# Performance work log

Measured on AMD Instinct MI355X. Metric: run time of the kernel, lower is better.

## Reference

```python
import jax, jax.numpy as jnp
import numpy as np

DIM = 1024
NUM_HEADS = 16
HEAD_DIM = DIM // NUM_HEADS
SCALE = HEAD_DIM ** -0.5


def setup_inputs() -> dict:
    key = jax.random.key(0)
    k1, k2, k3 = jax.random.split(key, 3)
    B, N = 4, 2048
    x = jax.random.normal(k1, (B, N, DIM), dtype=jnp.float32)
    w_qkv = jax.random.normal(k2, (DIM, 3 * DIM), dtype=jnp.float32) * (DIM ** -0.5)
    w_proj = jax.random.normal(k3, (DIM, DIM), dtype=jnp.float32) * (DIM ** -0.5)
    b_proj = jnp.zeros((DIM,), dtype=jnp.float32)
    return {"x": x, "w_qkv": w_qkv, "w_proj": w_proj, "b_proj": b_proj}


def reference(x, w_qkv, w_proj, b_proj):
    B, N, C = x.shape
    H, D = NUM_HEADS, HEAD_DIM
    # qkv projection: (B,N,3C) -> (3,B,H,N,D)
    qkv = (x @ w_qkv).reshape(B, N, 3, H, D).transpose(2, 0, 3, 1, 4)
    q, k, v = qkv[0], qkv[1], qkv[2]
    # full attention scores (B,H,N,N), scaled
    attn = jnp.einsum("bhnd,bhmd->bhnm", q, k) * SCALE
    attn = jax.nn.softmax(attn, axis=-1)
    out = jnp.einsum("bhnm,bhmd->bhnd", attn, v)
    out = out.transpose(0, 2, 1, 3).reshape(B, N, C)
    return out @ w_proj + b_proj
```

## Files before the change

### kernel.cpp

```cpp
#include <hip/hip_runtime.h>
#include <stdint.h>

#define DIM 1024
#define NHEADS 16
#define HDIM 64
#define BATCH 4
#define SEQ 2048
#define NTOK (BATCH*SEQ)
#define SCALE_L2E 0.1803368801111244f

typedef float f32x4  __attribute__((ext_vector_type(4)));
typedef short s16x8  __attribute__((ext_vector_type(8)));

#define MFMA16(a,b,c) __builtin_amdgcn_mfma_f32_16x16x32_bf16((a),(b),(c),0,0,0)

static __device__ __forceinline__ uint16_t f2bf(float f) {
    uint32_t u = __builtin_bit_cast(uint32_t, f);
    return (uint16_t)((u + 0x7FFFu + ((u >> 16) & 1u)) >> 16);
}

static __device__ __forceinline__ uint32_t cvt_pk_bf16(float lo, float hi) {
    uint32_t r;
    asm("v_cvt_pk_bf16_f32 %0, %1, %2" : "=v"(r) : "v"(lo), "v"(hi));
    return r;
}

static __device__ __forceinline__ void gl_lds16(const void* g, void* l) {
    __builtin_amdgcn_global_load_lds(
        (const __attribute__((address_space(1))) unsigned int*)g,
        (__attribute__((address_space(3))) unsigned int*)l, 16, 0, 0);
}

__global__ void convert_f32_bf16(const float* __restrict__ in, uint16_t* __restrict__ out) {
    const int i = blockIdx.x * blockDim.x + threadIdx.x;
    const float4 a = ((const float4*)in)[2*i];
    const float4 b = ((const float4*)in)[2*i + 1];
    ushort4 lo, hi;
    lo.x = f2bf(a.x); lo.y = f2bf(a.y); lo.z = f2bf(a.z); lo.w = f2bf(a.w);
    hi.x = f2bf(b.x); hi.y = f2bf(b.y); hi.z = f2bf(b.z); hi.w = f2bf(b.w);
    ((ushort4*)out)[2*i]     = lo;
    ((ushort4*)out)[2*i + 1] = hi;
}

__global__ void transpose_conv(const float* __restrict__ w, uint16_t* __restrict__ wT,
                               int K, int N) {
    __shared__ float t[32][33];
    const int tx = threadIdx.x, ty = threadIdx.y;
    const int n0 = blockIdx.x * 32, k0 = blockIdx.y * 32;
    #pragma unroll
    for (int i = 0; i < 4; ++i)
        t[ty + i*8][tx] = w[(size_t)(k0 + ty + i*8) * N + n0 + tx];
    __syncthreads();
    #pragma unroll
    for (int i = 0; i < 4; ++i)
        wT[(size_t)(n0 + ty + i*8) * K + k0 + tx] = f2bf(t[tx][ty + i*8]);
}

template <int MODE>
__global__ __launch_bounds__(256) void gemm_bt(
    const uint16_t* __restrict__ A, const uint16_t* __restrict__ B,
    void* __restrict__ C, const float* __restrict__ bias,
    int M, int N, int K)
{
    __shared__ uint16_t As[128*64];
    __shared__ uint16_t Bs[128*64];
    const int tid  = threadIdx.x;
    const int lane = tid & 63;
    const int wid  = tid >> 6;
    const int wm = wid >> 1, wn = wid & 1;
    const long row0 = (long)blockIdx.y * 128;
    const long col0 = (long)blockIdx.x * 128;

    const int sr  = lane >> 3;
    const int scb = (lane & 7) * 16;

    f32x4 acc[4][4] = {};

    for (int kt = 0; kt < K; kt += 64) {
        #pragma unroll
        for (int j = 0; j < 4; ++j) {
            const int r = (wid*4 + j)*8 + sr;
            const int c = (scb ^ ((r & 7) << 4)) >> 1;
            gl_lds16(&A[(row0 + r)*K + kt + c], &As[(wid*4 + j)*512]);
            gl_lds16(&B[(col0 + r)*K + kt + c], &Bs[(wid*4 + j)*512]);
        }
        __syncthreads();
        #pragma unroll
        for (int ks = 0; ks < 2; ++ks) {
            const int xb = (ks*32 + (lane >> 4)*8) * 2;
            s16x8 av[4], bv[4];
            #pragma unroll
            for (int f = 0; f < 4; ++f) {
                const int ra = wm*64 + f*16 + (lane & 15);
                av[f] = *(const s16x8*)((const char*)As + ra*128 + (xb ^ ((ra & 7) << 4)));
                const int rb = wn*64 + f*16 + (lane & 15);
                bv[f] = *(const s16x8*)((const char*)Bs + rb*128 + (xb ^ ((rb & 7) << 4)));
            }
            #pragma unroll
            for (int i = 0; i < 4; ++i)
                #pragma unroll
                for (int j = 0; j < 4; ++j)
                    acc[i][j] = MFMA16(av[i], bv[j], acc[i][j]);
        }
        __syncthreads();
    }

    #pragma unroll
    for (int i = 0; i < 4; ++i) {
        const long row = row0 + wm*64 + i*16 + (lane >> 4)*4;
        #pragma unroll
        for (int j = 0; j < 4; ++j) {
            const long col = col0 + wn*64 + j*16 + (lane & 15);
            #pragma unroll
            for (int r = 0; r < 4; ++r) {
                if (MODE == 0)
                    ((uint16_t*)C)[(row + r)*N + col] = f2bf(acc[i][j][r]);
                else
                    ((float*)C)[(row + r)*N + col] = acc[i][j][r] + bias[col];
            }
        }
    }
}

__global__ __launch_bounds__(512, 2) void qkv_gemm(
    const uint16_t* __restrict__ A, const uint16_t* __restrict__ B,
    uint16_t* __restrict__ Qb, uint16_t* __restrict__ Kb,
    uint16_t* __restrict__ VTb)
{
    __shared__ uint16_t As[2][256*64];
    __shared__ uint16_t Bs[2][192*64];
    const int tid = threadIdx.x, lane = tid & 63, wid = tid >> 6;
    const int wr = wid >> 2, wc = wid & 3;
    const int q15 = lane & 15, g = lane >> 4;

    int bid = blockIdx.y * gridDim.x + blockIdx.x;
    bid = (bid & 7) * 64 + (bid >> 3);
    const int  bx  = bid & 15;
    const long row0 = (long)(bid >> 4) * 256;
    const int  col0 = bx * 192;

    const int r_  = tid >> 3;
    const int sc  = (((tid & 7) * 16) ^ ((r_ & 7) << 4)) >> 1;

    f32x4 acc[8][3] = {};

#define QSTAGE(bf_, t_) do {                                                    \
    const int kt_ = (t_) * 64;                                                  \
    _Pragma("unroll")                                                           \
    for (int j_ = 0; j_ < 4; ++j_)                                              \
        gl_lds16(&A[(row0 + j_*64 + r_)*DIM + kt_ + sc], &As[bf_][j_*4096 + tid*8]); \
    _Pragma("unroll")                                                           \
    for (int j_ = 0; j_ < 3; ++j_)                                              \
        gl_lds16(&B[(size_t)(col0 + j_*64 + r_)*DIM + kt_ + sc], &Bs[bf_][j_*4096 + tid*8]); \
} while (0)

    QSTAGE(0, 0);

    for (int t = 0; t < 16; ++t) {
        const int p = t & 1;
        __syncthreads();
        QSTAGE(p ^ 1, (t < 15 ? t + 1 : 15));
        #pragma unroll
        for (int ks = 0; ks < 2; ++ks) {
            const int xb = (ks*32 + g*8) * 2;
            s16x8 av[8], bv[3];
            #pragma unroll
            for (int m = 0; m < 8; ++m) {
                const int ra = wr*128 + m*16 + q15;
                av[m] = *(const s16x8*)((const char*)As[p] + ra*128 + (xb ^ ((ra & 7) << 4)));
            }
            #pragma unroll
            for (int n = 0; n < 3; ++n) {
                const int rb = wc*48 + n*16 + q15;
                bv[n] = *(const s16x8*)((const char*)Bs[p] + rb*128 + (xb ^ ((rb & 7) << 4)));
            }
            #pragma unroll
            for (int m = 0; m < 8; ++m)
                #pragma unroll
                for (int n = 0; n < 3; ++n)
                    acc[m][n] = MFMA16(av[m], bv[n], acc[m][n]);
        }
    }
#undef QSTAGE

    #pragma unroll
    for (int n = 0; n < 3; ++n) {
        const int c = col0 + wc*48 + n*16 + q15;
        const int s = c >> 10;
        if (s == 2) {
            const int vrow = c - 2048;
            #pragma unroll
            for (int m = 0; m < 8; ++m) {
                const long rr = row0 + wr*128 + m*16 + g*4;
                uint2 w;
                w.x = cvt_pk_bf16(acc[m][n][0], acc[m][n][1]);
                w.y = cvt_pk_bf16(acc[m][n][2], acc[m][n][3]);
                *(uint2*)&VTb[(size_t)vrow*NTOK + rr] = w;
            }
        } else {
            uint16_t* dst = s ? Kb : Qb;
            const float scl = s ? 1.0f : SCALE_L2E;
            const int hd = (c >> 6) & 15, d = c & 63;
            #pragma unroll
            for (int m = 0; m < 8; ++m) {
                #pragma unroll
                for (int r = 0; r < 4; ++r) {
                    const long rr = row0 + wr*128 + m*16 + g*4 + r;
                    const int b = (int)(rr >> 11), nt = (int)(rr & 2047);
                    dst[((size_t)(b*NHEADS + hd)*SEQ + nt)*HDIM + d] = f2bf(acc[m][n][r] * scl);
                }
            }
        }
    }
}

__global__ __launch_bounds__(256) void attn_kernel(
    const uint16_t* __restrict__ Q, const uint16_t* __restrict__ Kg,
    const uint16_t* __restrict__ VT, uint16_t* __restrict__ O)
{
    __shared__ uint16_t Ks[2][64*64];
    __shared__ uint16_t Vs[2][64*64];
    __shared__ uint16_t Ps[128*64];
    const int tid = threadIdx.x, lane = tid & 63, wid = tid >> 6;
    const int bid = blockIdx.x;
    const int xcd = bid & 7, idx = bid >> 3;
    const int bh = xcd*8 + (idx >> 4);
    const int qt = idx & 15;
    const int b = bh >> 4, h = bh & 15;
    const uint16_t* Qh = Q  + (size_t)bh * SEQ * HDIM;
    const uint16_t* Kh = Kg + (size_t)bh * SEQ * HDIM;
    const uint16_t* Vh = VT + (size_t)h * HDIM * NTOK + (size_t)b * SEQ;
    const int qbase = qt*128 + wid*32;
    const int g = lane >> 4, q15 = lane & 15;
    const int swl = (lane & 7) << 4;

    s16x8 bq[2][2];
    #pragma unroll
    for (int i = 0; i < 2; ++i)
        #pragma unroll
        for (int ks = 0; ks < 2; ++ks)
            bq[i][ks] = *(const s16x8*)&Qh[(size_t)(qbase + i*16 + q15)*HDIM + ks*32 + g*8];

    f32x4 o[2][4] = {};
    f32x4 lacc[2] = {};

    const int sr  = lane >> 3;
    const int scb = (lane & 7) * 16;
    const int stg_c = (scb ^ (sr << 4)) >> 1;

    #define STAGE(bf, t)                                                          \
        _Pragma("unroll")                                                         \
        for (int j = 0; j < 2; ++j) {                                             \
            const int r = (wid*2 + j)*8 + sr;                                     \
            gl_lds16(&Kh[(size_t)((t)*64 + r)*HDIM + stg_c], &Ks[bf][(wid*2 + j)*512]); \
            gl_lds16(&Vh[(size_t)r*NTOK + (t)*64 + stg_c],   &Vs[bf][(wid*2 + j)*512]); \
        }

    STAGE(0, 0)
    __syncthreads();

    for (int it = 0; it < 32; ++it) {
        const int cur = it & 1;
        if (it < 31) STAGE(cur ^ 1, it + 1)

        const char* ksb = (const char*)Ks[cur];
        const char* vsb = (const char*)Vs[cur];

        f32x4 st[2][4] = {};
        #pragma unroll
        for (int ks = 0; ks < 2; ++ks) {
            const int xb = (ks*32 + g*8) * 2;
            s16x8 ak[4];
            #pragma unroll
            for (int f = 0; f < 4; ++f) {
                const int rk = f*16 + q15;
                ak[f] = *(const s16x8*)(ksb + rk*128 + (xb ^ ((rk & 7) << 4)));
            }
            #pragma unroll
            for (int i = 0; i < 2; ++i)
                #pragma unroll
                for (int f = 0; f < 4; ++f)
                    st[i][f] = MFMA16(ak[f], bq[i][ks], st[i][f]);
        }

        #pragma unroll
        for (int i = 0; i < 2; ++i) {
            #pragma unroll
            for (int f = 0; f < 4; ++f) {
                #pragma unroll
                for (int r = 0; r < 4; ++r)
                    st[i][f][r] = __builtin_amdgcn_exp2f(st[i][f][r]);
            }
            lacc[i] += (st[i][0] + st[i][1]) + (st[i][2] + st[i][3]);
        }

        #pragma unroll
        for (int i = 0; i < 2; ++i) {
            char* base = (char*)Ps + (wid*32 + i*16 + q15)*128;
            #pragma unroll
            for (int f = 0; f < 4; ++f) {
                uint2 w;
                w.x = cvt_pk_bf16(st[i][f][0], st[i][f][1]);
                w.y = cvt_pk_bf16(st[i][f][2], st[i][f][3]);
                *(uint2*)(base + ((f*32 + g*8) ^ swl)) = w;
            }
        }

        #pragma unroll
        for (int ks = 0; ks < 2; ++ks) {
            s16x8 pa[2], vb[4];
            #pragma unroll
            for (int i = 0; i < 2; ++i)
                pa[i] = *(const s16x8*)((const char*)Ps + (wid*32 + i*16 + q15)*128
                                         + ((ks*64 + g*16) ^ swl));
            const int xbv = (ks*32 + g*8) * 2;
            #pragma unroll
            for (int f = 0; f < 4; ++f) {
                const int rv = f*16 + q15;
                vb[f] = *(const s16x8*)(vsb + rv*128 + (xbv ^ ((rv & 7) << 4)));
            }
            #pragma unroll
            for (int i = 0; i < 2; ++i)
                #pragma unroll
                for (int f = 0; f < 4; ++f)
                    o[i][f] = MFMA16(pa[i], vb[f], o[i][f]);
        }

        __syncthreads();
    }
    #undef STAGE

    #pragma unroll
    for (int i = 0; i < 2; ++i) {
        float ls = (lacc[i][0] + lacc[i][1]) + (lacc[i][2] + lacc[i][3]);
        ls += __shfl_xor(ls, 16);
        ls += __shfl_xor(ls, 32);
        #pragma unroll
        for (int r = 0; r < 4; ++r) {
            const float l_r = __shfl(ls, g*4 + r);
            const float inv = 1.0f / l_r;
            const int n = qbase + i*16 + g*4 + r;
            const size_t base = ((size_t)b*SEQ + n)*DIM + h*HDIM;
            #pragma unroll
            for (int f = 0; f < 4; ++f)
                O[base + f*16 + q15] = f2bf(o[i][f][r] * inv);
        }
    }
}

extern "C" void kernel_launch(void* const* d_in, const int* in_sizes, int n_in,
                              void* d_out, int out_size, void* d_ws, size_t ws_size,
                              hipStream_t stream)
{
    const float* x      = (const float*)d_in[0];
    const float* w_qkv  = (const float*)d_in[1];
    const float* w_proj = (const float*)d_in[2];
    const float* b_proj = (const float*)d_in[3];
    float* out = (float*)d_out;

    uint16_t* xb     = (uint16_t*)d_ws;
    uint16_t* wqkvT  = xb     + (size_t)NTOK*DIM;
    uint16_t* wprojT = wqkvT  + (size_t)3*DIM*DIM;
    uint16_t* Qb     = wprojT + (size_t)DIM*DIM;
    uint16_t* Kb     = Qb     + (size_t)NTOK*DIM;
    uint16_t* VTb    = Kb     + (size_t)NTOK*DIM;
    uint16_t* attn_o = VTb    + (size_t)NTOK*DIM;

    convert_f32_bf16<<<dim3(NTOK*DIM/8/256), dim3(256), 0, stream>>>(x, xb);
    transpose_conv<<<dim3(96, 32), dim3(32, 8), 0, stream>>>(w_qkv, wqkvT, DIM, 3*DIM);
    transpose_conv<<<dim3(32, 32), dim3(32, 8), 0, stream>>>(w_proj, wprojT, DIM, DIM);
    qkv_gemm<<<dim3(16, 32), dim3(512), 0, stream>>>(xb, wqkvT, Qb, Kb, VTb);
    attn_kernel<<<dim3(1024), dim3(256), 0, stream>>>(Qb, Kb, VTb, attn_o);
    gemm_bt<1><<<dim3(8, 64), dim3(256), 0, stream>>>(attn_o, wprojT, out, b_proj, NTOK, DIM, DIM);
}
```

Measured before the change: 199.4 us.

## Merge weight transposes, enlarge attention blocks, add double-buffered projection GEMM

Merges the two weight transpose launches into one kernel. The attention kernel now uses 512-thread blocks covering 256 queries each, so every K/V tile staged in shared memory serves twice as many queries and each thread issues a single staging load. The generic output-projection GEMM is replaced by a 256x128-tile kernel that double-buffers its shared-memory tiles. The qkv_gemm launch bound drops its min-blocks hint, so the compiler may use more registers at the cost of fewer resident blocks. The larger tiles cut global traffic but halve the block count to 512 for attention and 256 for projection, which may reduce occupancy.

Result: faster. 187.2 us (-6.1%).

```diff
diff --git a/kernel.cpp b/kernel.cpp
--- a/kernel.cpp
+++ b/kernel.cpp
@@ -42,87 +42,25 @@
     ((ushort4*)out)[2*i + 1] = hi;
 }
 
-__global__ void transpose_conv(const float* __restrict__ w, uint16_t* __restrict__ wT,
-                               int K, int N) {
+__global__ void transpose_conv2(const float* __restrict__ w_qkv, uint16_t* __restrict__ wqkvT,
+                                const float* __restrict__ w_proj, uint16_t* __restrict__ wprojT) {
     __shared__ float t[32][33];
     const int tx = threadIdx.x, ty = threadIdx.y;
-    const int n0 = blockIdx.x * 32, k0 = blockIdx.y * 32;
+    const int bx = blockIdx.x;
+    const float* w; uint16_t* wT; int N, n0;
+    if (bx < 96) { w = w_qkv;  wT = wqkvT;  N = 3*DIM; n0 = bx * 32; }
+    else         { w = w_proj; wT = wprojT; N = DIM;   n0 = (bx - 96) * 32; }
+    const int k0 = blockIdx.y * 32;
     #pragma unroll
     for (int i = 0; i < 4; ++i)
         t[ty + i*8][tx] = w[(size_t)(k0 + ty + i*8) * N + n0 + tx];
     __syncthreads();
     #pragma unroll
     for (int i = 0; i < 4; ++i)
-        wT[(size_t)(n0 + ty + i*8) * K + k0 + tx] = f2bf(t[tx][ty + i*8]);
-}
-
-template <int MODE>
-__global__ __launch_bounds__(256) void gemm_bt(
-    const uint16_t* __restrict__ A, const uint16_t* __restrict__ B,
-    void* __restrict__ C, const float* __restrict__ bias,
-    int M, int N, int K)
-{
-    __shared__ uint16_t As[128*64];
-    __shared__ uint16_t Bs[128*64];
-    const int tid  = threadIdx.x;
-    const int lane = tid & 63;
-    const int wid  = tid >> 6;
-    const int wm = wid >> 1, wn = wid & 1;
-    const long row0 = (long)blockIdx.y * 128;
-    const long col0 = (long)blockIdx.x * 128;
-
-    const int sr  = lane >> 3;
-    const int scb = (lane & 7) * 16;
-
-    f32x4 acc[4][4] = {};
-
-    for (int kt = 0; kt < K; kt += 64) {
-        #pragma unroll
-        for (int j = 0; j < 4; ++j) {
-            const int r = (wid*4 + j)*8 + sr;
-            const int c = (scb ^ ((r & 7) << 4)) >> 1;
-            gl_lds16(&A[(row0 + r)*K + kt + c], &As[(wid*4 + j)*512]);
-            gl_lds16(&B[(col0 + r)*K + kt + c], &Bs[(wid*4 + j)*512]);
-        }
-        __syncthreads();
-        #pragma unroll
-        for (int ks = 0; ks < 2; ++ks) {
-            const int xb = (ks*32 + (lane >> 4)*8) * 2;
-            s16x8 av[4], bv[4];
-            #pragma unroll
-            for (int f = 0; f < 4; ++f) {
-                const int ra = wm*64 + f*16 + (lane & 15);
-                av[f] = *(const s16x8*)((const char*)As + ra*128 + (xb ^ ((ra & 7) << 4)));
-                const int rb = wn*64 + f*16 + (lane & 15);
-                bv[f] = *(const s16x8*)((const char*)Bs + rb*128 + (xb ^ ((rb & 7) << 4)));
-            }
-            #pragma unroll
-            for (int i = 0; i < 4; ++i)
-                #pragma unroll
-                for (int j = 0; j < 4; ++j)
-                    acc[i][j] = MFMA16(av[i], bv[j], acc[i][j]);
-        }
-        __syncthreads();
-    }
-
-    #pragma unroll
-    for (int i = 0; i < 4; ++i) {
-        const long row = row0 + wm*64 + i*16 + (lane >> 4)*4;
-        #pragma unroll
-        for (int j = 0; j < 4; ++j) {
-            const long col = col0 + wn*64 + j*16 + (lane & 15);
-            #pragma unroll
-            for (int r = 0; r < 4; ++r) {
-                if (MODE == 0)
-                    ((uint16_t*)C)[(row + r)*N + col] = f2bf(acc[i][j][r]);
-                else
-                    ((float*)C)[(row + r)*N + col] = acc[i][j][r] + bias[col];
-            }
-        }
-    }
-}
-
-__global__ __launch_bounds__(512, 2) void qkv_gemm(
+        wT[(size_t)(n0 + ty + i*8) * DIM + k0 + tx] = f2bf(t[tx][ty + i*8]);
+}
+
+__global__ __launch_bounds__(512) void qkv_gemm(
     const uint16_t* __restrict__ A, const uint16_t* __restrict__ B,
     uint16_t* __restrict__ Qb, uint16_t* __restrict__ Kb,
     uint16_t* __restrict__ VTb)
@@ -214,23 +152,93 @@
     }
 }
 
-__global__ __launch_bounds__(256) void attn_kernel(
+__global__ __launch_bounds__(512) void gemm_proj(
+    const uint16_t* __restrict__ A, const uint16_t* __restrict__ B,
+    float* __restrict__ C, const float* __restrict__ bias)
+{
+    __shared__ uint16_t As[2][256*64];
+    __shared__ uint16_t Bs[2][128*64];
+    const int tid = threadIdx.x, lane = tid & 63, wid = tid >> 6;
+    const int wr = wid >> 2, wc = wid & 3;
+    const int q15 = lane & 15, g = lane >> 4;
+    const long row0 = (long)blockIdx.y * 256;
+    const int  col0 = blockIdx.x * 128;
+
+    const int r_  = tid >> 3;
+    const int sc  = (((tid & 7) * 16) ^ ((r_ & 7) << 4)) >> 1;
+
+    f32x4 acc[8][2] = {};
+
+#define PSTAGE(bf_, t_) do {                                                    \
+    const int kt_ = (t_) * 64;                                                  \
+    _Pragma("unroll")                                                           \
+    for (int j_ = 0; j_ < 4; ++j_)                                              \
+        gl_lds16(&A[(row0 + j_*64 + r_)*DIM + kt_ + sc], &As[bf_][j_*4096 + tid*8]); \
+    _Pragma("unroll")                                                           \
+    for (int j_ = 0; j_ < 2; ++j_)                                              \
+        gl_lds16(&B[(size_t)(col0 + j_*64 + r_)*DIM + kt_ + sc], &Bs[bf_][j_*4096 + tid*8]); \
+} while (0)
+
+    PSTAGE(0, 0);
+
+    for (int t = 0; t < 16; ++t) {
+        const int p = t & 1;
+        __syncthreads();
+        PSTAGE(p ^ 1, (t < 15 ? t + 1 : 15));
+        #pragma unroll
+        for (int ks = 0; ks < 2; ++ks) {
+            const int xb = (ks*32 + g*8) * 2;
+            s16x8 av[8], bv[2];
+            #pragma unroll
+            for (int m = 0; m < 8; ++m) {
+                const int ra = wr*128 + m*16 + q15;
+                av[m] = *(const s16x8*)((const char*)As[p] + ra*128 + (xb ^ ((ra & 7) << 4)));
+            }
+            #pragma unroll
+            for (int n = 0; n < 2; ++n) {
+                const int rb = wc*32 + n*16 + q15;
+                bv[n] = *(const s16x8*)((const char*)Bs[p] + rb*128 + (xb ^ ((rb & 7) << 4)));
+            }
+            #pragma unroll
+            for (int m = 0; m < 8; ++m)
+                #pragma unroll
+                for (int n = 0; n < 2; ++n)
+                    acc[m][n] = MFMA16(av[m], bv[n], acc[m][n]);
+        }
+    }
+#undef PSTAGE
+
+    #pragma unroll
+    for (int n = 0; n < 2; ++n) {
+        const int col = col0 + wc*32 + n*16 + q15;
+        const float bval = bias[col];
+        #pragma unroll
+        for (int m = 0; m < 8; ++m) {
+            const long row = row0 + wr*128 + m*16 + g*4;
+            #pragma unroll
+            for (int r = 0; r < 4; ++r)
+                C[(row + r)*DIM + col] = acc[m][n][r] + bval;
+        }
+    }
+}
+
+__global__ __launch_bounds__(512) void attn_kernel(
     const uint16_t* __restrict__ Q, const uint16_t* __restrict__ Kg,
     const uint16_t* __restrict__ VT, uint16_t* __restrict__ O)
 {
     __shared__ uint16_t Ks[2][64*64];
     __shared__ uint16_t Vs[2][64*64];
-    __shared__ uint16_t Ps[128*64];
+    __shared__ uint16_t Ps[256*64];
     const int tid = threadIdx.x, lane = tid & 63, wid = tid >> 6;
     const int bid = blockIdx.x;
     const int xcd = bid & 7, idx = bid >> 3;
-    const int bh = xcd*8 + (idx >> 4);
-    const int qt = idx & 15;
+    const int bh = xcd*8 + (idx >> 3);
+    const int qt = idx & 7;
     const int b = bh >> 4, h = bh & 15;
     const uint16_t* Qh = Q  + (size_t)bh * SEQ * HDIM;
     const uint16_t* Kh = Kg + (size_t)bh * SEQ * HDIM;
     const uint16_t* Vh = VT + (size_t)h * HDIM * NTOK + (size_t)b * SEQ;
-    const int qbase = qt*128 + wid*32;
+    const int qbase = qt*256 + wid*32;
     const int g = lane >> 4, q15 = lane & 15;
     const int swl = (lane & 7) << 4;
 
@@ -244,24 +252,20 @@
     f32x4 o[2][4] = {};
     f32x4 lacc[2] = {};
 
-    const int sr  = lane >> 3;
-    const int scb = (lane & 7) * 16;
-    const int stg_c = (scb ^ (sr << 4)) >> 1;
-
-    #define STAGE(bf, t)                                                          \
-        _Pragma("unroll")                                                         \
-        for (int j = 0; j < 2; ++j) {                                             \
-            const int r = (wid*2 + j)*8 + sr;                                     \
-            gl_lds16(&Kh[(size_t)((t)*64 + r)*HDIM + stg_c], &Ks[bf][(wid*2 + j)*512]); \
-            gl_lds16(&Vh[(size_t)r*NTOK + (t)*64 + stg_c],   &Vs[bf][(wid*2 + j)*512]); \
-        }
-
-    STAGE(0, 0)
+    const int r_  = tid >> 3;
+    const int stg_c = (((tid & 7) * 16) ^ ((r_ & 7) << 4)) >> 1;
+
+    #define STAGE(bf, t) do {                                                 \
+        gl_lds16(&Kh[(size_t)((t)*64 + r_)*HDIM + stg_c], &Ks[bf][tid*8]);    \
+        gl_lds16(&Vh[(size_t)r_*NTOK + (t)*64 + stg_c],   &Vs[bf][tid*8]);    \
+    } while (0)
+
+    STAGE(0, 0);
     __syncthreads();
 
     for (int it = 0; it < 32; ++it) {
         const int cur = it & 1;
-        if (it < 31) STAGE(cur ^ 1, it + 1)
+        if (it < 31) STAGE(cur ^ 1, it + 1);
 
         const char* ksb = (const char*)Ks[cur];
         const char* vsb = (const char*)Vs[cur];
@@ -367,9 +371,8 @@
     uint16_t* attn_o = VTb    + (size_t)NTOK*DIM;
 
     convert_f32_bf16<<<dim3(NTOK*DIM/8/256), dim3(256), 0, stream>>>(x, xb);
-    transpose_conv<<<dim3(96, 32), dim3(32, 8), 0, stream>>>(w_qkv, wqkvT, DIM, 3*DIM);
-    transpose_conv<<<dim3(32, 32), dim3(32, 8), 0, stream>>>(w_proj, wprojT, DIM, DIM);
+    transpose_conv2<<<dim3(128, 32), dim3(32, 8), 0, stream>>>(w_qkv, wqkvT, w_proj, wprojT);
     qkv_gemm<<<dim3(16, 32), dim3(512), 0, stream>>>(xb, wqkvT, Qb, Kb, VTb);
-    attn_kernel<<<dim3(1024), dim3(256), 0, stream>>>(Qb, Kb, VTb, attn_o);
-    gemm_bt<1><<<dim3(8, 64), dim3(256), 0, stream>>>(attn_o, wprojT, out, b_proj, NTOK, DIM, DIM);
-}
+    attn_kernel<<<dim3(512), dim3(512), 0, stream>>>(Qb, Kb, VTb, attn_o);
+    gemm_proj<<<dim3(8, 32), dim3(512), 0, stream>>>(attn_o, wprojT, out, b_proj);
+}
```

## Retile QKV GEMM, double-buffer projection GEMM, merge weight transposes, shrink P buffer

Applied to the files above, without the earlier changes.

The QKV GEMM moves from 256x192 tiles with 512 threads to 128x128 tiles with 256 threads and an XCD-aware block remap, and it no longer issues a redundant final prefetch. The output projection GEMM becomes a dedicated kernel with double-buffered LDS staging, XCD swizzling and a bias value hoisted per column. The two weight transpose launches are merged into one. The attention kernel writes and reads P in two halves through a buffer half the size, dropping the XOR swizzle on it, which may bring LDS bank conflicts back.

Result: slower. 258.3 us (+29.5%).

```diff
diff --git a/kernel.cpp b/kernel.cpp
--- a/kernel.cpp
+++ b/kernel.cpp
@@ -42,159 +42,94 @@
     ((ushort4*)out)[2*i + 1] = hi;
 }
 
-__global__ void transpose_conv(const float* __restrict__ w, uint16_t* __restrict__ wT,
-                               int K, int N) {
+__global__ void transpose_conv2(const float* __restrict__ w_qkv, uint16_t* __restrict__ wqkvT,
+                                const float* __restrict__ w_proj, uint16_t* __restrict__ wprojT) {
     __shared__ float t[32][33];
     const int tx = threadIdx.x, ty = threadIdx.y;
-    const int n0 = blockIdx.x * 32, k0 = blockIdx.y * 32;
+    const int bx = blockIdx.x;
+    const float* w; uint16_t* wT; int N, n0;
+    if (bx < 96) { w = w_qkv;  wT = wqkvT;  N = 3*DIM; n0 = bx * 32; }
+    else         { w = w_proj; wT = wprojT; N = DIM;   n0 = (bx - 96) * 32; }
+    const int k0 = blockIdx.y * 32;
     #pragma unroll
     for (int i = 0; i < 4; ++i)
         t[ty + i*8][tx] = w[(size_t)(k0 + ty + i*8) * N + n0 + tx];
     __syncthreads();
     #pragma unroll
     for (int i = 0; i < 4; ++i)
-        wT[(size_t)(n0 + ty + i*8) * K + k0 + tx] = f2bf(t[tx][ty + i*8]);
-}
-
-template <int MODE>
-__global__ __launch_bounds__(256) void gemm_bt(
-    const uint16_t* __restrict__ A, const uint16_t* __restrict__ B,
-    void* __restrict__ C, const float* __restrict__ bias,
-    int M, int N, int K)
-{
-    __shared__ uint16_t As[128*64];
-    __shared__ uint16_t Bs[128*64];
-    const int tid  = threadIdx.x;
-    const int lane = tid & 63;
-    const int wid  = tid >> 6;
-    const int wm = wid >> 1, wn = wid & 1;
-    const long row0 = (long)blockIdx.y * 128;
-    const long col0 = (long)blockIdx.x * 128;
-
-    const int sr  = lane >> 3;
-    const int scb = (lane & 7) * 16;
-
-    f32x4 acc[4][4] = {};
-
-    for (int kt = 0; kt < K; kt += 64) {
-        #pragma unroll
-        for (int j = 0; j < 4; ++j) {
-            const int r = (wid*4 + j)*8 + sr;
-            const int c = (scb ^ ((r & 7) << 4)) >> 1;
-            gl_lds16(&A[(row0 + r)*K + kt + c], &As[(wid*4 + j)*512]);
-            gl_lds16(&B[(col0 + r)*K + kt + c], &Bs[(wid*4 + j)*512]);
-        }
-        __syncthreads();
-        #pragma unroll
-        for (int ks = 0; ks < 2; ++ks) {
-            const int xb = (ks*32 + (lane >> 4)*8) * 2;
-            s16x8 av[4], bv[4];
-            #pragma unroll
-            for (int f = 0; f < 4; ++f) {
-                const int ra = wm*64 + f*16 + (lane & 15);
-                av[f] = *(const s16x8*)((const char*)As + ra*128 + (xb ^ ((ra & 7) << 4)));
-                const int rb = wn*64 + f*16 + (lane & 15);
-                bv[f] = *(const s16x8*)((const char*)Bs + rb*128 + (xb ^ ((rb & 7) << 4)));
-            }
-            #pragma unroll
-            for (int i = 0; i < 4; ++i)
-                #pragma unroll
-                for (int j = 0; j < 4; ++j)
-                    acc[i][j] = MFMA16(av[i], bv[j], acc[i][j]);
-        }
-        __syncthreads();
-    }
-
-    #pragma unroll
-    for (int i = 0; i < 4; ++i) {
-        const long row = row0 + wm*64 + i*16 + (lane >> 4)*4;
-        #pragma unroll
-        for (int j = 0; j < 4; ++j) {
-            const long col = col0 + wn*64 + j*16 + (lane & 15);
-            #pragma unroll
-            for (int r = 0; r < 4; ++r) {
-                if (MODE == 0)
-                    ((uint16_t*)C)[(row + r)*N + col] = f2bf(acc[i][j][r]);
-                else
-                    ((float*)C)[(row + r)*N + col] = acc[i][j][r] + bias[col];
-            }
-        }
-    }
-}
-
-__global__ __launch_bounds__(512, 2) void qkv_gemm(
+        wT[(size_t)(n0 + ty + i*8) * DIM + k0 + tx] = f2bf(t[tx][ty + i*8]);
+}
+
+__global__ __launch_bounds__(256) void qkv_gemm(
     const uint16_t* __restrict__ A, const uint16_t* __restrict__ B,
     uint16_t* __restrict__ Qb, uint16_t* __restrict__ Kb,
     uint16_t* __restrict__ VTb)
 {
-    __shared__ uint16_t As[2][256*64];
-    __shared__ uint16_t Bs[2][192*64];
+    __shared__ uint16_t As[2][128*64];
+    __shared__ uint16_t Bs[2][128*64];
     const int tid = threadIdx.x, lane = tid & 63, wid = tid >> 6;
-    const int wr = wid >> 2, wc = wid & 3;
+    const int wm = wid >> 1, wn = wid & 1;
     const int q15 = lane & 15, g = lane >> 4;
 
-    int bid = blockIdx.y * gridDim.x + blockIdx.x;
-    bid = (bid & 7) * 64 + (bid >> 3);
-    const int  bx  = bid & 15;
-    const long row0 = (long)(bid >> 4) * 256;
-    const int  col0 = bx * 192;
-
-    const int r_  = tid >> 3;
-    const int sc  = (((tid & 7) * 16) ^ ((r_ & 7) << 4)) >> 1;
-
-    f32x4 acc[8][3] = {};
-
-#define QSTAGE(bf_, t_) do {                                                    \
+    const int bid = blockIdx.x;
+    const int sb  = (bid & 7) * 192 + (bid >> 3);
+    const int ct  = sb >> 6;
+    const long row0 = (long)(sb & 63) * 128;
+    const int  col0 = ct * 128;
+
+    const int sr    = lane >> 3;
+    const int stg_c = (((lane & 7) * 16) ^ (sr << 4)) >> 1;
+
+    f32x4 acc[4][4] = {};
+
+#define QS(bf_, t_) do {                                                        \
     const int kt_ = (t_) * 64;                                                  \
     _Pragma("unroll")                                                           \
-    for (int j_ = 0; j_ < 4; ++j_)                                              \
-        gl_lds16(&A[(row0 + j_*64 + r_)*DIM + kt_ + sc], &As[bf_][j_*4096 + tid*8]); \
-    _Pragma("unroll")                                                           \
-    for (int j_ = 0; j_ < 3; ++j_)                                              \
-        gl_lds16(&B[(size_t)(col0 + j_*64 + r_)*DIM + kt_ + sc], &Bs[bf_][j_*4096 + tid*8]); \
+    for (int j_ = 0; j_ < 4; ++j_) {                                            \
+        const int r_ = (wid*4 + j_)*8 + sr;                                     \
+        gl_lds16(&A[(row0 + r_)*DIM + kt_ + stg_c], &As[bf_][(wid*4 + j_)*512]); \
+        gl_lds16(&B[(size_t)(col0 + r_)*DIM + kt_ + stg_c], &Bs[bf_][(wid*4 + j_)*512]); \
+    }                                                                           \
 } while (0)
 
-    QSTAGE(0, 0);
+    QS(0, 0);
 
     for (int t = 0; t < 16; ++t) {
         const int p = t & 1;
         __syncthreads();
-        QSTAGE(p ^ 1, (t < 15 ? t + 1 : 15));
+        if (t < 15) QS(p ^ 1, t + 1);
         #pragma unroll
         for (int ks = 0; ks < 2; ++ks) {
             const int xb = (ks*32 + g*8) * 2;
-            s16x8 av[8], bv[3];
-            #pragma unroll
-            for (int m = 0; m < 8; ++m) {
-                const int ra = wr*128 + m*16 + q15;
-                av[m] = *(const s16x8*)((const char*)As[p] + ra*128 + (xb ^ ((ra & 7) << 4)));
-            }
-            #pragma unroll
-            for (int n = 0; n < 3; ++n) {
-                const int rb = wc*48 + n*16 + q15;
-                bv[n] = *(const s16x8*)((const char*)Bs[p] + rb*128 + (xb ^ ((rb & 7) << 4)));
-            }
-            #pragma unroll
-            for (int m = 0; m < 8; ++m)
-                #pragma unroll
-                for (int n = 0; n < 3; ++n)
-                    acc[m][n] = MFMA16(av[m], bv[n], acc[m][n]);
-        }
-    }
-#undef QSTAGE
-
-    #pragma unroll
-    for (int n = 0; n < 3; ++n) {
-        const int c = col0 + wc*48 + n*16 + q15;
+            s16x8 av[4], bv[4];
+            #pragma unroll
+            for (int f = 0; f < 4; ++f) {
+                const int ra = wm*64 + f*16 + q15;
+                av[f] = *(const s16x8*)((const char*)As[p] + ra*128 + (xb ^ ((ra & 7) << 4)));
+                const int rb = wn*64 + f*16 + q15;
+                bv[f] = *(const s16x8*)((const char*)Bs[p] + rb*128 + (xb ^ ((rb & 7) << 4)));
+            }
+            #pragma unroll
+            for (int i = 0; i < 4; ++i)
+                #pragma unroll
+                for (int j = 0; j < 4; ++j)
+                    acc[i][j] = MFMA16(av[i], bv[j], acc[i][j]);
+        }
+    }
+#undef QS
+
+    #pragma unroll
+    for (int j = 0; j < 4; ++j) {
+        const int c = col0 + wn*64 + j*16 + q15;
         const int s = c >> 10;
         if (s == 2) {
             const int vrow = c - 2048;
             #pragma unroll
-            for (int m = 0; m < 8; ++m) {
-                const long rr = row0 + wr*128 + m*16 + g*4;
+            for (int i = 0; i < 4; ++i) {
+                const long rr = row0 + wm*64 + i*16 + g*4;
                 uint2 w;
-                w.x = cvt_pk_bf16(acc[m][n][0], acc[m][n][1]);
-                w.y = cvt_pk_bf16(acc[m][n][2], acc[m][n][3]);
+                w.x = cvt_pk_bf16(acc[i][j][0], acc[i][j][1]);
+                w.y = cvt_pk_bf16(acc[i][j][2], acc[i][j][3]);
                 *(uint2*)&VTb[(size_t)vrow*NTOK + rr] = w;
             }
         } else {
@@ -202,14 +137,84 @@
             const float scl = s ? 1.0f : SCALE_L2E;
             const int hd = (c >> 6) & 15, d = c & 63;
             #pragma unroll
-            for (int m = 0; m < 8; ++m) {
+            for (int i = 0; i < 4; ++i) {
                 #pragma unroll
                 for (int r = 0; r < 4; ++r) {
-                    const long rr = row0 + wr*128 + m*16 + g*4 + r;
+                    const long rr = row0 + wm*64 + i*16 + g*4 + r;
                     const int b = (int)(rr >> 11), nt = (int)(rr & 2047);
-                    dst[((size_t)(b*NHEADS + hd)*SEQ + nt)*HDIM + d] = f2bf(acc[m][n][r] * scl);
+                    dst[((size_t)(b*NHEADS + hd)*SEQ + nt)*HDIM + d] = f2bf(acc[i][j][r] * scl);
                 }
             }
+        }
+    }
+}
+
+__global__ __launch_bounds__(256) void gemm_proj(
+    const uint16_t* __restrict__ A, const uint16_t* __restrict__ B,
+    float* __restrict__ C, const float* __restrict__ bias)
+{
+    __shared__ uint16_t As[2][128*64];
+    __shared__ uint16_t Bs[2][128*64];
+    const int tid = threadIdx.x, lane = tid & 63, wid = tid >> 6;
+    const int wm = wid >> 1, wn = wid & 1;
+    const int q15 = lane & 15, g = lane >> 4;
+
+    const int bid = blockIdx.x;
+    const int sb  = (bid & 7) * 64 + (bid >> 3);
+    const long row0 = (long)(sb & 63) * 128;
+    const int  col0 = (sb >> 6) * 128;
+
+    const int sr    = lane >> 3;
+    const int stg_c = (((lane & 7) * 16) ^ (sr << 4)) >> 1;
+
+    f32x4 acc[4][4] = {};
+
+#define PS(bf_, t_) do {                                                        \
+    const int kt_ = (t_) * 64;                                                  \
+    _Pragma("unroll")                                                           \
+    for (int j_ = 0; j_ < 4; ++j_) {                                            \
+        const int r_ = (wid*4 + j_)*8 + sr;                                     \
+        gl_lds16(&A[(row0 + r_)*DIM + kt_ + stg_c], &As[bf_][(wid*4 + j_)*512]); \
+        gl_lds16(&B[(size_t)(col0 + r_)*DIM + kt_ + stg_c], &Bs[bf_][(wid*4 + j_)*512]); \
+    }                                                                           \
+} while (0)
+
+    PS(0, 0);
+
+    for (int t = 0; t < 16; ++t) {
+        const int p = t & 1;
+        __syncthreads();
+        if (t < 15) PS(p ^ 1, t + 1);
+        #pragma unroll
+        for (int ks = 0; ks < 2; ++ks) {
+            const int xb = (ks*32 + g*8) * 2;
+            s16x8 av[4], bv[4];
+            #pragma unroll
+            for (int f = 0; f < 4; ++f) {
+                const int ra = wm*64 + f*16 + q15;
+                av[f] = *(const s16x8*)((const char*)As[p] + ra*128 + (xb ^ ((ra & 7) << 4)));
+                const int rb = wn*64 + f*16 + q15;
+                bv[f] = *(const s16x8*)((const char*)Bs[p] + rb*128 + (xb ^ ((rb & 7) << 4)));
+            }
+            #pragma unroll
+            for (int i = 0; i < 4; ++i)
+                #pragma unroll
+                for (int j = 0; j < 4; ++j)
+                    acc[i][j] = MFMA16(av[i], bv[j], acc[i][j]);
+        }
+    }
+#undef PS
+
+    #pragma unroll
+    for (int j = 0; j < 4; ++j) {
+        const int col = col0 + wn*64 + j*16 + q15;
+        const float bval = bias[col];
+        #pragma unroll
+        for (int i = 0; i < 4; ++i) {
+            const long row = row0 + wm*64 + i*16 + g*4;
+            #pragma unroll
+            for (int r = 0; r < 4; ++r)
+                C[(row + r)*DIM + col] = acc[i][j][r] + bval;
         }
     }
 }
@@ -220,7 +225,7 @@
 {
     __shared__ uint16_t Ks[2][64*64];
     __shared__ uint16_t Vs[2][64*64];
-    __shared__ uint16_t Ps[128*64];
+    __shared__ uint16_t Ps[128*32];
     const int tid = threadIdx.x, lane = tid & 63, wid = tid >> 6;
     const int bid = blockIdx.x;
     const int xcd = bid & 7, idx = bid >> 3;
@@ -232,7 +237,6 @@
     const uint16_t* Vh = VT + (size_t)h * HDIM * NTOK + (size_t)b * SEQ;
     const int qbase = qt*128 + wid*32;
     const int g = lane >> 4, q15 = lane & 15;
-    const int swl = (lane & 7) << 4;
 
     s16x8 bq[2][2];
     #pragma unroll
@@ -244,9 +248,8 @@
     f32x4 o[2][4] = {};
     f32x4 lacc[2] = {};
 
-    const int sr  = lane >> 3;
-    const int scb = (lane & 7) * 16;
-    const int stg_c = (scb ^ (sr << 4)) >> 1;
+    const int sr    = lane >> 3;
+    const int stg_c = (((lane & 7) * 16) ^ (sr << 4)) >> 1;
 
     #define STAGE(bf, t)                                                          \
         _Pragma("unroll")                                                         \
@@ -295,25 +298,24 @@
         }
 
         #pragma unroll
-        for (int i = 0; i < 2; ++i) {
-            char* base = (char*)Ps + (wid*32 + i*16 + q15)*128;
-            #pragma unroll
-            for (int f = 0; f < 4; ++f) {
-                uint2 w;
-                w.x = cvt_pk_bf16(st[i][f][0], st[i][f][1]);
-                w.y = cvt_pk_bf16(st[i][f][2], st[i][f][3]);
-                *(uint2*)(base + ((f*32 + g*8) ^ swl)) = w;
-            }
-        }
-
-        #pragma unroll
-        for (int ks = 0; ks < 2; ++ks) {
+        for (int hf = 0; hf < 2; ++hf) {
+            #pragma unroll
+            for (int i = 0; i < 2; ++i) {
+                char* base = (char*)Ps + (wid*32 + i*16 + q15)*64;
+                #pragma unroll
+                for (int fh = 0; fh < 2; ++fh) {
+                    const int f = 2*hf + fh;
+                    uint2 w;
+                    w.x = cvt_pk_bf16(st[i][f][0], st[i][f][1]);
+                    w.y = cvt_pk_bf16(st[i][f][2], st[i][f][3]);
+                    *(uint2*)(base + fh*32 + g*8) = w;
+                }
+            }
             s16x8 pa[2], vb[4];
             #pragma unroll
             for (int i = 0; i < 2; ++i)
-                pa[i] = *(const s16x8*)((const char*)Ps + (wid*32 + i*16 + q15)*128
-                                         + ((ks*64 + g*16) ^ swl));
-            const int xbv = (ks*32 + g*8) * 2;
+                pa[i] = *(const s16x8*)((const char*)Ps + (wid*32 + i*16 + q15)*64 + g*16);
+            const int xbv = (hf*32 + g*8) * 2;
             #pragma unroll
             for (int f = 0; f < 4; ++f) {
                 const int rv = f*16 + q15;
@@ -367,9 +369,8 @@
     uint16_t* attn_o = VTb    + (size_t)NTOK*DIM;
 
     convert_f32_bf16<<<dim3(NTOK*DIM/8/256), dim3(256), 0, stream>>>(x, xb);
-    transpose_conv<<<dim3(96, 32), dim3(32, 8), 0, stream>>>(w_qkv, wqkvT, DIM, 3*DIM);
-    transpose_conv<<<dim3(32, 32), dim3(32, 8), 0, stream>>>(w_proj, wprojT, DIM, DIM);
-    qkv_gemm<<<dim3(16, 32), dim3(512), 0, stream>>>(xb, wqkvT, Qb, Kb, VTb);
+    transpose_conv2<<<dim3(128, 32), dim3(32, 8), 0, stream>>>(w_qkv, wqkvT, w_proj, wprojT);
+    qkv_gemm<<<dim3(1536), dim3(256), 0, stream>>>(xb, wqkvT, Qb, Kb, VTb);
     attn_kernel<<<dim3(1024), dim3(256), 0, stream>>>(Qb, Kb, VTb, attn_o);
-    gemm_bt<1><<<dim3(8, 64), dim3(256), 0, stream>>>(attn_o, wprojT, out, b_proj, NTOK, DIM, DIM);
-}
+    gemm_proj<<<dim3(512), dim3(256), 0, stream>>>(attn_o, wprojT, out, b_proj);
+}
```
